# Performance work log

Measured on AMD Instinct MI355X. Metric: run time of the kernel, lower is better.

## Reference

```python
import jax, jax.numpy as jnp
import numpy as np

B, D, K, E = 256, 256, 1024, 16  # batch, dim_codes, book_size, embedding_dim
DECAY = 0.999
GAIN = 1.0 - DECAY
EPS = 1e-6


def setup_inputs() -> dict:
    key = jax.random.key(0)
    k1, k2 = jax.random.split(key)
    return {
        "cw_q": jax.random.normal(k1, (B, D * E), dtype=jnp.float32),
        "codebook": jax.random.normal(k2, (D, K, E), dtype=jnp.float32),
        "ema_counts": jnp.ones((D, K), dtype=jnp.float32),
    }


def reference(cw_q, codebook, ema_counts):
    batch = cw_q.shape[0]
    x = cw_q.reshape(batch, D, E)  # [B, D, E]

    x2 = jnp.sum(x * x, axis=-1)                       # [B, D]
    c2 = jnp.sum(codebook * codebook, axis=-1)         # [D, K]
    xc = jnp.einsum('bde,dke->bdk', x, codebook)       # [B, D, K]
    dist = x2[:, :, None] + c2[None, :, :] - 2.0 * xc

    idx = jnp.argmin(dist, axis=-1)                    # [B, D] int32

    # gather nearest code vector per (batch, dim_code)
    cw_embed = codebook[jnp.arange(D)[None, :], idx]   # [B, D, E]
    cw_embed = cw_embed.reshape(batch, D * E)

    one_hot_idx = jax.nn.one_hot(idx, K, dtype=cw_q.dtype)  # [B, D, K]

    # EMA update (training path): scatter-sum of assigned vectors per code
    update = jnp.einsum('bdk,bde->dke', one_hot_idx, x)      # [D, K, E]
    new_codebook = codebook * DECAY + GAIN * update / (ema_counts[:, :, None] + EPS)
    new_ema_counts = DECAY * ema_counts + GAIN * jnp.sum(one_hot_idx, axis=0)

    return cw_embed, one_hot_idx, new_codebook, new_ema_counts
```

## Files before the change

### kernel.cpp

```cpp
#include <hip/hip_runtime.h>

#define BB 256
#define DD 256
#define KK 1024
#define EE 16
#define DECAY 0.999f
#define GAIN  0.001f
#define EPS   1e-6f

#define OH_OFF   ((size_t)BB * DD * EE)
#define CB_OFF   (OH_OFF + (size_t)BB * DD * KK)
#define EMA_OFF  (CB_OFF + (size_t)DD * KK * EE)

__device__ __forceinline__ float dot16(const float4& a0, const float4& a1,
                                       const float4& a2, const float4& a3,
                                       const float4& b0, const float4& b1,
                                       const float4& b2, const float4& b3) {
  float s = a0.x * b0.x;
  s = fmaf(a0.y, b0.y, s); s = fmaf(a0.z, b0.z, s); s = fmaf(a0.w, b0.w, s);
  s = fmaf(a1.x, b1.x, s); s = fmaf(a1.y, b1.y, s); s = fmaf(a1.z, b1.z, s); s = fmaf(a1.w, b1.w, s);
  s = fmaf(a2.x, b2.x, s); s = fmaf(a2.y, b2.y, s); s = fmaf(a2.z, b2.z, s); s = fmaf(a2.w, b2.w, s);
  s = fmaf(a3.x, b3.x, s); s = fmaf(a3.y, b3.y, s); s = fmaf(a3.z, b3.z, s); s = fmaf(a3.w, b3.w, s);
  return s;
}

__global__ __launch_bounds__(256) void vqvae_fused(
    const float* __restrict__ cw_q,
    const float* __restrict__ codebook,
    const float* __restrict__ ema,
    float* __restrict__ out)
{
  __shared__ float4 cb4s[KK * EE / 4];
  __shared__ float4 upd4s[KK * EE / 4];
  __shared__ float  c2s[KK];
  __shared__ float  cnts[KK];
  __shared__ float  pbest[2 * BB];
  __shared__ int    pidx[2 * BB];

  float* upd = (float*)upd4s;

  const int t = threadIdx.x;
  const int d = blockIdx.x;
  const float4 z4 = make_float4(0.f, 0.f, 0.f, 0.f);

  #pragma unroll
  for (int j = 0; j < 4; ++j) { c2s[t + 256 * j] = 0.f; cnts[t + 256 * j] = 0.f; }
  #pragma unroll
  for (int i = 0; i < 16; ++i) upd4s[i * 256 + t] = z4;
  __syncthreads();

  const float4* src4 = (const float4*)codebook + (size_t)d * (KK * EE / 4);
  #pragma unroll
  for (int i = 0; i < 16; ++i) {
    int idx4 = i * 256 + t;
    float4 v = src4[idx4];
    cb4s[idx4] = v;
    float sq = fmaf(v.x, v.x, 0.f);
    sq = fmaf(v.y, v.y, sq); sq = fmaf(v.z, v.z, sq); sq = fmaf(v.w, v.w, sq);
    atomicAdd(&c2s[idx4 >> 2], sq);
  }
  __syncthreads();

  const int h  = t >> 7;
  const int b0 = (t & 127) << 1;
  const int b1 = b0 + 1;

  const float4* xr0 = (const float4*)cw_q + (size_t)b0 * (DD * EE / 4) + d * 4;
  const float4* xr1 = (const float4*)cw_q + (size_t)b1 * (DD * EE / 4) + d * 4;
  float4 xa0 = xr0[0], xb0 = xr0[1], xc0 = xr0[2], xd0 = xr0[3];
  float4 xa1 = xr1[0], xb1 = xr1[1], xc1 = xr1[2], xd1 = xr1[3];
  const float x2_0 = dot16(xa0, xb0, xc0, xd0, xa0, xb0, xc0, xd0);
  const float x2_1 = dot16(xa1, xb1, xc1, xd1, xa1, xb1, xc1, xd1);

  float best0 = 3.4e38f, best1 = 3.4e38f;
  int   bi0 = 0, bi1 = 0;
  const int kbase = h << 9;

  float* ohp = out + OH_OFF;
  const int w = t >> 6;
  const int l = t & 63;

  for (int s = 0; s < 256; ++s) {
    const int k0 = kbase + (s << 1);
    const int k1 = k0 + 1;
    const float4* p = cb4s + (k0 << 2);
    float4 ca0 = p[0], ca1 = p[1], ca2 = p[2], ca3 = p[3];
    float4 cb0 = p[4], cb1 = p[5], cb2 = p[6], cb3 = p[7];

    float dot00 = dot16(ca0, ca1, ca2, ca3, xa0, xb0, xc0, xd0);
    float dot01 = dot16(ca0, ca1, ca2, ca3, xa1, xb1, xc1, xd1);
    float dot10 = dot16(cb0, cb1, cb2, cb3, xa0, xb0, xc0, xd0);
    float dot11 = dot16(cb0, cb1, cb2, cb3, xa1, xb1, xc1, xd1);

    const float c2k0 = c2s[k0], c2k1 = c2s[k1];
    float d00 = (x2_0 + c2k0) - 2.f * dot00;
    if (d00 < best0) { best0 = d00; bi0 = k0; }
    float d01 = (x2_1 + c2k0) - 2.f * dot01;
    if (d01 < best1) { best1 = d01; bi1 = k0; }
    float d10 = (x2_0 + c2k1) - 2.f * dot10;
    if (d10 < best0) { best0 = d10; bi0 = k1; }
    float d11 = (x2_1 + c2k1) - 2.f * dot11;
    if (d11 < best1) { best1 = d11; bi1 = k1; }

    const int brow = (w << 6) + (s >> 2);
    const int q = s & 3;
    float4* dst = (float4*)(ohp + (size_t)brow * (DD * KK) + (size_t)d * KK + q * 256);
    dst[l] = z4;
  }

  pbest[(h << 8) + b0] = best0;  pidx[(h << 8) + b0] = bi0;
  pbest[(h << 8) + b1] = best1;  pidx[(h << 8) + b1] = bi1;
  __syncthreads();

  {
    const int b = t;
    float e0 = pbest[b];        int i0 = pidx[b];
    float e1 = pbest[256 + b];  int i1 = pidx[256 + b];
    const int bidx = (e1 < e0) ? i1 : i0;

    float4* ce = (float4*)out + (size_t)b * (DD * EE / 4) + d * 4;
    const float4* cw = cb4s + (bidx << 2);
    ce[0] = cw[0]; ce[1] = cw[1]; ce[2] = cw[2]; ce[3] = cw[3];

    ohp[(size_t)b * (DD * KK) + (size_t)d * KK + bidx] = 1.0f;

    atomicAdd(&cnts[bidx], 1.0f);
    const float* xrow = cw_q + (size_t)b * (DD * EE) + (size_t)d * EE;
    #pragma unroll
    for (int e = 0; e < 16; ++e) atomicAdd(&upd[(bidx << 4) + e], xrow[e]);
  }
  __syncthreads();

  float* ema_sh = c2s;
  const float* emad   = ema + (size_t)d * KK;
  float* out_ema      = out + EMA_OFF + (size_t)d * KK;
  #pragma unroll
  for (int j = 0; j < 4; ++j) {
    int k = t + 256 * j;
    float ev = emad[k];
    ema_sh[k] = ev;
    out_ema[k] = DECAY * ev + GAIN * cnts[k];
  }
  __syncthreads();

  float4* out_cb4 = (float4*)(out + CB_OFF) + (size_t)d * (KK * EE / 4);
  #pragma unroll
  for (int i = 0; i < 16; ++i) {
    int idx4 = i * 256 + t;
    int k = idx4 >> 2;
    float4 c = cb4s[idx4];
    float4 u = upd4s[idx4];
    float inv = GAIN / (ema_sh[k] + EPS);
    float4 r;
    r.x = DECAY * c.x + u.x * inv;
    r.y = DECAY * c.y + u.y * inv;
    r.z = DECAY * c.z + u.z * inv;
    r.w = DECAY * c.w + u.w * inv;
    out_cb4[idx4] = r;
  }
}

extern "C" void kernel_launch(void* const* d_in, const int* in_sizes, int n_in,
                              void* d_out, int out_size, void* d_ws, size_t ws_size,
                              hipStream_t stream) {
  const float* cw_q     = (const float*)d_in[0];
  const float* codebook = (const float*)d_in[1];
  const float* ema      = (const float*)d_in[2];
  float* out = (float*)d_out;
  (void)in_sizes; (void)n_in; (void)out_size; (void)d_ws; (void)ws_size;
  vqvae_fused<<<dim3(DD), dim3(256), 0, stream>>>(cw_q, codebook, ema, out);
}
```

Before: 320.9 us.

## Split fused VQ kernel into assign and update kernels with doubled grid

Splits the single fused kernel into an assignment kernel over 512 blocks (two batch halves per code dimension) and a separate EMA update kernel that reads indices from workspace. The assign kernel drops the large update buffer from shared memory so two blocks can share a CU, and it reduces per-code norms with shuffles instead of shared atomics. This is meant to raise occupancy and parallelism for the compute-and-zero-fill phase. In exchange it adds a second launch, a workspace round trip, and reloads the codebook from global memory in the update kernel.

```diff
diff --git a/kernel.cpp b/kernel.cpp
--- a/kernel.cpp
+++ b/kernel.cpp
@@ -1,4 +1,5 @@
 #include <hip/hip_runtime.h>
+#include <float.h>
 
 #define BB 256
 #define DD 256
@@ -24,139 +25,169 @@
   return s;
 }
 
-__global__ __launch_bounds__(256) void vqvae_fused(
+__global__ __launch_bounds__(256, 2) void vq_assign(
     const float* __restrict__ cw_q,
     const float* __restrict__ codebook,
-    const float* __restrict__ ema,
-    float* __restrict__ out)
+    float* __restrict__ out,
+    int* __restrict__ idx_ws)
 {
   __shared__ float4 cb4s[KK * EE / 4];
-  __shared__ float4 upd4s[KK * EE / 4];
   __shared__ float  c2s[KK];
-  __shared__ float  cnts[KK];
-  __shared__ float  pbest[2 * BB];
-  __shared__ int    pidx[2 * BB];
-
-  float* upd = (float*)upd4s;
-
-  const int t = threadIdx.x;
-  const int d = blockIdx.x;
-  const float4 z4 = make_float4(0.f, 0.f, 0.f, 0.f);
-
-  #pragma unroll
-  for (int j = 0; j < 4; ++j) { c2s[t + 256 * j] = 0.f; cnts[t + 256 * j] = 0.f; }
-  #pragma unroll
-  for (int i = 0; i < 16; ++i) upd4s[i * 256 + t] = z4;
-  __syncthreads();
-
-  const float4* src4 = (const float4*)codebook + (size_t)d * (KK * EE / 4);
-  #pragma unroll
-  for (int i = 0; i < 16; ++i) {
-    int idx4 = i * 256 + t;
-    float4 v = src4[idx4];
-    cb4s[idx4] = v;
-    float sq = fmaf(v.x, v.x, 0.f);
-    sq = fmaf(v.y, v.y, sq); sq = fmaf(v.z, v.z, sq); sq = fmaf(v.w, v.w, sq);
-    atomicAdd(&c2s[idx4 >> 2], sq);
-  }
-  __syncthreads();
-
-  const int h  = t >> 7;
-  const int b0 = (t & 127) << 1;
-  const int b1 = b0 + 1;
-
+  __shared__ float  pbest[4 * 128];
+  __shared__ int    pidxs[4 * 128];
+
+  const int t  = threadIdx.x;
+  const int d  = blockIdx.x >> 1;
+  const int hf = blockIdx.x & 1;
+  const int w  = t >> 6;
+  const int l  = t & 63;
+
+  const int b0 = hf * 128 + l;
+  const int b1 = b0 + 64;
   const float4* xr0 = (const float4*)cw_q + (size_t)b0 * (DD * EE / 4) + d * 4;
   const float4* xr1 = (const float4*)cw_q + (size_t)b1 * (DD * EE / 4) + d * 4;
   float4 xa0 = xr0[0], xb0 = xr0[1], xc0 = xr0[2], xd0 = xr0[3];
   float4 xa1 = xr1[0], xb1 = xr1[1], xc1 = xr1[2], xd1 = xr1[3];
+
+  const float4* src4 = (const float4*)codebook + (size_t)d * (KK * EE / 4);
+  #pragma unroll
+  for (int i = 0; i < 16; ++i) {
+    int i4 = i * 256 + t;
+    float4 v = src4[i4];
+    cb4s[i4] = v;
+    float sq = v.x * v.x;
+    sq = fmaf(v.y, v.y, sq);
+    sq = fmaf(v.z, v.z, sq);
+    sq = fmaf(v.w, v.w, sq);
+    sq += __shfl_xor(sq, 1);
+    sq += __shfl_xor(sq, 2);
+    if ((t & 3) == 0) c2s[i4 >> 2] = sq;
+  }
+  __syncthreads();
+
   const float x2_0 = dot16(xa0, xb0, xc0, xd0, xa0, xb0, xc0, xd0);
   const float x2_1 = dot16(xa1, xb1, xc1, xd1, xa1, xb1, xc1, xd1);
 
-  float best0 = 3.4e38f, best1 = 3.4e38f;
+  float best0 = FLT_MAX, best1 = FLT_MAX;
   int   bi0 = 0, bi1 = 0;
-  const int kbase = h << 9;
-
-  float* ohp = out + OH_OFF;
-  const int w = t >> 6;
-  const int l = t & 63;
-
+  const int kbase = w << 8;
+
+  float2* zbase = (float2*)(out + OH_OFF + (size_t)(hf * 128) * (DD * KK)
+                            + (size_t)d * KK + kbase) + l;
+
+  #pragma unroll 2
   for (int s = 0; s < 256; ++s) {
-    const int k0 = kbase + (s << 1);
-    const int k1 = k0 + 1;
-    const float4* p = cb4s + (k0 << 2);
-    float4 ca0 = p[0], ca1 = p[1], ca2 = p[2], ca3 = p[3];
-    float4 cb0 = p[4], cb1 = p[5], cb2 = p[6], cb3 = p[7];
-
-    float dot00 = dot16(ca0, ca1, ca2, ca3, xa0, xb0, xc0, xd0);
-    float dot01 = dot16(ca0, ca1, ca2, ca3, xa1, xb1, xc1, xd1);
-    float dot10 = dot16(cb0, cb1, cb2, cb3, xa0, xb0, xc0, xd0);
-    float dot11 = dot16(cb0, cb1, cb2, cb3, xa1, xb1, xc1, xd1);
-
-    const float c2k0 = c2s[k0], c2k1 = c2s[k1];
-    float d00 = (x2_0 + c2k0) - 2.f * dot00;
-    if (d00 < best0) { best0 = d00; bi0 = k0; }
-    float d01 = (x2_1 + c2k0) - 2.f * dot01;
-    if (d01 < best1) { best1 = d01; bi1 = k0; }
-    float d10 = (x2_0 + c2k1) - 2.f * dot10;
-    if (d10 < best0) { best0 = d10; bi0 = k1; }
-    float d11 = (x2_1 + c2k1) - 2.f * dot11;
-    if (d11 < best1) { best1 = d11; bi1 = k1; }
-
-    const int brow = (w << 6) + (s >> 2);
-    const int q = s & 3;
-    float4* dst = (float4*)(ohp + (size_t)brow * (DD * KK) + (size_t)d * KK + q * 256);
-    dst[l] = z4;
-  }
-
-  pbest[(h << 8) + b0] = best0;  pidx[(h << 8) + b0] = bi0;
-  pbest[(h << 8) + b1] = best1;  pidx[(h << 8) + b1] = bi1;
+    const int k = kbase + s;
+    const float4* p = cb4s + (k << 2);
+    float4 c0 = p[0], c1 = p[1], c2v = p[2], c3 = p[3];
+
+    float dot0 = dot16(c0, c1, c2v, c3, xa0, xb0, xc0, xd0);
+    float dot1 = dot16(c0, c1, c2v, c3, xa1, xb1, xc1, xd1);
+    const float c2k = c2s[k];
+    float d0 = fmaf(-2.f, dot0, x2_0 + c2k);
+    float d1 = fmaf(-2.f, dot1, x2_1 + c2k);
+    if (d0 < best0) { best0 = d0; bi0 = k; }
+    if (d1 < best1) { best1 = d1; bi1 = k; }
+
+    const int r  = s >> 1;
+    const int hh = s & 1;
+    zbase[(size_t)r * (DD * KK / 2) + hh * 64] = make_float2(0.f, 0.f);
+  }
+
+  pbest[w * 128 + l]      = best0;  pidxs[w * 128 + l]      = bi0;
+  pbest[w * 128 + l + 64] = best1;  pidxs[w * 128 + l + 64] = bi1;
+  __syncthreads();
+
+  if (t < 128) {
+    float bb = pbest[t];
+    int   bi = pidxs[t];
+    #pragma unroll
+    for (int w2 = 1; w2 < 4; ++w2) {
+      float e = pbest[w2 * 128 + t];
+      int   ii = pidxs[w2 * 128 + t];
+      if (e < bb) { bb = e; bi = ii; }
+    }
+    const int b = hf * 128 + t;
+
+    float4* ce = (float4*)out + (size_t)b * (DD * EE / 4) + d * 4;
+    const float4* cw = cb4s + (bi << 2);
+    ce[0] = cw[0]; ce[1] = cw[1]; ce[2] = cw[2]; ce[3] = cw[3];
+
+    out[OH_OFF + (size_t)b * (DD * KK) + (size_t)d * KK + bi] = 1.0f;
+
+    idx_ws[d * BB + b] = bi;
+  }
+}
+
+__global__ __launch_bounds__(256) void vq_update(
+    const float* __restrict__ cw_q,
+    const float* __restrict__ codebook,
+    const float* __restrict__ ema,
+    const int* __restrict__ idx_ws,
+    float* __restrict__ out)
+{
+  __shared__ float upds[KK * EE];
+  __shared__ float cnts[KK];
+  __shared__ float esh[KK];
+  __shared__ int   ish[BB];
+
+  const int t = threadIdx.x;
+  const int d = blockIdx.x;
+  float4* upd4 = (float4*)upds;
+  const float4 z4 = make_float4(0.f, 0.f, 0.f, 0.f);
+
+  #pragma unroll
+  for (int i = 0; i < 16; ++i) upd4[i * 256 + t] = z4;
+  #pragma unroll
+  for (int j = 0; j < 4; ++j) cnts[t + 256 * j] = 0.f;
   __syncthreads();
 
   {
-    const int b = t;
-    float e0 = pbest[b];        int i0 = pidx[b];
-    float e1 = pbest[256 + b];  int i1 = pidx[256 + b];
-    const int bidx = (e1 < e0) ? i1 : i0;
-
-    float4* ce = (float4*)out + (size_t)b * (DD * EE / 4) + d * 4;
-    const float4* cw = cb4s + (bidx << 2);
-    ce[0] = cw[0]; ce[1] = cw[1]; ce[2] = cw[2]; ce[3] = cw[3];
-
-    ohp[(size_t)b * (DD * KK) + (size_t)d * KK + bidx] = 1.0f;
-
-    atomicAdd(&cnts[bidx], 1.0f);
-    const float* xrow = cw_q + (size_t)b * (DD * EE) + (size_t)d * EE;
+    int kidx = idx_ws[d * BB + t];
+    ish[t] = kidx;
+    atomicAdd(&cnts[kidx], 1.0f);
+  }
+  __syncthreads();
+
+  {
+    const int e = t & 15;
+    const int g = t >> 4;
     #pragma unroll
-    for (int e = 0; e < 16; ++e) atomicAdd(&upd[(bidx << 4) + e], xrow[e]);
-  }
-  __syncthreads();
-
-  float* ema_sh = c2s;
-  const float* emad   = ema + (size_t)d * KK;
-  float* out_ema      = out + EMA_OFF + (size_t)d * KK;
+    for (int i = 0; i < 16; ++i) {
+      int b = g * 16 + i;
+      int k = ish[b];
+      float xv = cw_q[(size_t)b * (DD * EE) + (size_t)d * EE + e];
+      atomicAdd(&upds[k * EE + e], xv);
+    }
+  }
+  __syncthreads();
+
+  const float* emad = ema + (size_t)d * KK;
+  float* out_ema    = out + EMA_OFF + (size_t)d * KK;
   #pragma unroll
   for (int j = 0; j < 4; ++j) {
     int k = t + 256 * j;
     float ev = emad[k];
-    ema_sh[k] = ev;
+    esh[k] = ev;
     out_ema[k] = DECAY * ev + GAIN * cnts[k];
   }
   __syncthreads();
 
-  float4* out_cb4 = (float4*)(out + CB_OFF) + (size_t)d * (KK * EE / 4);
+  const float4* cb4 = (const float4*)codebook + (size_t)d * (KK * EE / 4);
+  float4* ocb4      = (float4*)(out + CB_OFF) + (size_t)d * (KK * EE / 4);
   #pragma unroll
   for (int i = 0; i < 16; ++i) {
-    int idx4 = i * 256 + t;
-    int k = idx4 >> 2;
-    float4 c = cb4s[idx4];
-    float4 u = upd4s[idx4];
-    float inv = GAIN / (ema_sh[k] + EPS);
+    int i4 = i * 256 + t;
+    int k  = i4 >> 2;
+    float4 c = cb4[i4];
+    float4 u = upd4[i4];
+    float inv = GAIN / (esh[k] + EPS);
     float4 r;
     r.x = DECAY * c.x + u.x * inv;
     r.y = DECAY * c.y + u.y * inv;
     r.z = DECAY * c.z + u.z * inv;
     r.w = DECAY * c.w + u.w * inv;
-    out_cb4[idx4] = r;
+    ocb4[i4] = r;
   }
 }
 
@@ -166,7 +197,10 @@
   const float* cw_q     = (const float*)d_in[0];
   const float* codebook = (const float*)d_in[1];
   const float* ema      = (const float*)d_in[2];
-  float* out = (float*)d_out;
-  (void)in_sizes; (void)n_in; (void)out_size; (void)d_ws; (void)ws_size;
-  vqvae_fused<<<dim3(DD), dim3(256), 0, stream>>>(cw_q, codebook, ema, out);
-}
+  float* out  = (float*)d_out;
+  int* idx_ws = (int*)d_ws;
+  (void)in_sizes; (void)n_in; (void)out_size; (void)ws_size;
+
+  vq_assign<<<dim3(512), dim3(256), 0, stream>>>(cw_q, codebook, out, idx_ws);
+  vq_update<<<dim3(256), dim3(256), 0, stream>>>(cw_q, codebook, ema, idx_ws, out);
+}
```

Measured after the change: 327.5 us. 2.1% more time.
